# Performance work log

Hardware: AMD Instinct MI355X
Metric: run time of the kernel (lower is better)

Reference implementation:

```python
import jax, jax.numpy as jnp
import numpy as np

B = 16384      # samples
NN = 11        # causal-graph nodes per sample (adult)
D = 4          # per-node raw feature dim (node_dim_max)
F = 32         # dim_input_enc = h_dim_list_enc[0]
EDIM = 4       # edge_dim
NI = 3         # number of intervention features

_BASE_EDGES = np.array([[0,3],[0,4],[1,3],[1,5],[2,5],[0,6],[3,6],[4,7],[5,7],
                        [6,8],[7,8],[2,9],[8,9],[3,10],[6,10],[9,10],[1,10]], dtype=np.int64)


def setup_inputs() -> dict:
    key = jax.random.key(0)
    ks = jax.random.split(key, 14)
    # batched edge index: replicate the 17-edge DAG per sample with node offsets
    off = (np.arange(B) * NN)[:, None]                      # [B,1]
    src = (_BASE_EDGES[:, 0][None, :] + off).reshape(-1).astype(np.int32)  # [E]
    dst = (_BASE_EDGES[:, 1][None, :] + off).reshape(-1).astype(np.int32)
    E = src.shape[0]
    g = lambda k, shp, s: jax.random.normal(k, shp, dtype=jnp.float32) * s
    return {
        'x_input':  g(ks[0], (B, NN * D), 1.0),
        'edge_attr': g(ks[1], (E, EDIM), 1.0),
        'W_emb':   g(ks[2], (NN, D, F), 1.0 / np.sqrt(D)),
        'b_emb':   jnp.zeros((NN, F), jnp.float32),
        'W_pre1':  g(ks[3], (NI, 2 * F + EDIM, F), 1.0 / np.sqrt(2 * F + EDIM)),
        'b_pre1':  jnp.zeros((NI, F), jnp.float32),
        'W_post1': g(ks[4], (NI, 12 * F, F), 1.0 / np.sqrt(12 * F)),
        'b_post1': jnp.zeros((NI, F), jnp.float32),
        'W_pre2':  g(ks[5], (NI, 2 * F + EDIM, F), 1.0 / np.sqrt(2 * F + EDIM)),
        'b_pre2':  jnp.zeros((NI, F), jnp.float32),
        'W_post2': g(ks[6], (NI, 12 * F, 1), 1.0 / np.sqrt(12 * F)),
        'b_post2': jnp.zeros((NI, 1), jnp.float32),
        'W_fc':    g(ks[7], (NI, NN, 1), 1.0 / np.sqrt(NN)),
        'b_fc':    jnp.zeros((NI, 1), jnp.float32),
        'edge_src': jnp.asarray(src),
        'edge_dst': jnp.asarray(dst),
    }


def _pna_conv(h, src, dst, e, Wpre, bpre, Wpost, bpost, cnt_c, mask, amp, att, N):
    # message: pre-MLP over [h_dst, h_src, edge_attr]
    m = jax.nn.relu(jnp.concatenate([h[dst], h[src], e], axis=1) @ Wpre + bpre)  # [E,F]
    s = jax.ops.segment_sum(m, dst, num_segments=N)
    mean = s / cnt_c[:, None]
    mean_sq = jax.ops.segment_sum(m * m, dst, num_segments=N) / cnt_c[:, None]
    std = jnp.sqrt(jax.nn.relu(mean_sq - mean * mean) + 1e-5)
    mn = jnp.where(mask[:, None], jax.ops.segment_min(m, dst, num_segments=N), 0.0)
    mx = jnp.where(mask[:, None], jax.ops.segment_max(m, dst, num_segments=N), 0.0)
    agg = jnp.concatenate([mean, mn, mx, std], axis=1)                 # [N,4F]
    scaled = jnp.concatenate([agg, agg * amp[:, None], agg * att[:, None]], axis=1)  # [N,12F]
    return scaled @ Wpost + bpost


def reference(x_input, edge_attr, W_emb, b_emb,
              W_pre1, b_pre1, W_post1, b_post1,
              W_pre2, b_pre2, W_post2, b_post2,
              W_fc, b_fc, edge_src, edge_dst):
    N = B * NN
    # encoder embeddings: per-node linear + relu (shared across interventions)
    X = x_input.reshape(B, NN, D)
    H = jax.nn.relu(jnp.einsum('bnd,ndf->bnf', X, W_emb) + b_emb).reshape(N, F)
    # degree stats for PNA scalers (in-degree)
    cnt = jax.ops.segment_sum(jnp.ones_like(edge_dst, dtype=jnp.float32), edge_dst, num_segments=N)
    mask = cnt > 0
    cnt_c = jnp.maximum(cnt, 1.0)
    logd = jnp.log1p(jnp.maximum(cnt, 1.0))
    avg_log = jnp.mean(logd)
    amp = logd / avg_log
    att = avg_log / logd
    outs = []
    for i in range(NI):
        h1 = jax.nn.relu(_pna_conv(H, edge_src, edge_dst, edge_attr,
                                   W_pre1[i], b_pre1[i], W_post1[i], b_post1[i],
                                   cnt_c, mask, amp, att, N))
        h2 = _pna_conv(h1, edge_src, edge_dst, edge_attr,
                       W_pre2[i], b_pre2[i], W_post2[i], b_post2[i],
                       cnt_c, mask, amp, att, N)            # [N,1]
        p = jax.nn.sigmoid(h2)                               # get_prob=True
        pm = p.reshape(B, NN).mean(axis=0)                   # return_mean=True -> [11]
        outs.append(pm @ W_fc[i] + b_fc[i])                  # [1]
    # padded sum over interventions == concatenation when inter_features == intervention_features
    return jnp.concatenate(outs)[None, :]                    # [1, NI]
```

## Files before the change

### kernel.cpp

```cpp
#include <hip/hip_runtime.h>
#include <math.h>

#define B_TOT   16384
#define SB      6
#define TPB     512

#define SSTRIDE 1652
#define OFF_H   0
#define OFF_EA  396
#define OFF_H1  464
#define OFF_AGG 860
#define OFF_TD  OFF_AGG
#define OFF_TS  (OFF_AGG + 396)
#define OFF_A4  600
#define OFF_A10 640
#define WLDS    (SB * SSTRIDE)

#define LW_B4   0
#define LW_H1C  32
#define LW_V1C1 64
#define LW_V10  160
#define LW_V4   288
#define LW_C42  320
#define LW_TSC  324
#define LW_BP1  356
#define LW_EA1  388
#define LW_EA2  516
#define LW_WC1  644
#define LTAB    3716

#define OFF_PACC (WLDS + LTAB)
#define LDS_FLOATS (WLDS + LTAB + 16)
#define AVG_LOG 0.9976091242438673f

#define G_WC1  0
#define G_W10  3072
#define G_W4   7168
#define G_SM   8192
#define WTAB   8548
#define WS_TAB 64

__constant__ int C_ESRC[17] = {0,0,1,1,2,0,3,4,5,6,7,2,8,3,6,9,1};
__constant__ int C1EA[6] = {0,3,5,7,9,11};
__constant__ int C1EB[6] = {2,4,6,8,10,12};
__constant__ int C1N[6]  = {3,5,6,7,8,9};

#define FMA16(a, wb, u) do { \
    float4 w0_ = *(const float4*)(wb); \
    float4 w1_ = *(const float4*)((wb) + 32); \
    float4 w2_ = *(const float4*)((wb) + 64); \
    float4 w3_ = *(const float4*)((wb) + 96); \
    u.x = fmaf(a.x, w0_.x, u.x); u.y = fmaf(a.x, w0_.y, u.y); u.z = fmaf(a.x, w0_.z, u.z); u.w = fmaf(a.x, w0_.w, u.w); \
    u.x = fmaf(a.y, w1_.x, u.x); u.y = fmaf(a.y, w1_.y, u.y); u.z = fmaf(a.y, w1_.z, u.z); u.w = fmaf(a.y, w1_.w, u.w); \
    u.x = fmaf(a.z, w2_.x, u.x); u.y = fmaf(a.z, w2_.y, u.y); u.z = fmaf(a.z, w2_.z, u.z); u.w = fmaf(a.z, w2_.w, u.w); \
    u.x = fmaf(a.w, w3_.x, u.x); u.y = fmaf(a.w, w3_.y, u.y); u.z = fmaf(a.w, w3_.z, u.z); u.w = fmaf(a.w, w3_.w, u.w); \
} while (0)

#define MSG(e_, m_) do { \
    const float4 ev_ = *(const float4*)(S + OFF_EA + (e_) * 4); \
    const float4 ts_ = *(const float4*)(S + OFF_TS + C_ESRC[(e_)] * 36 + f); \
    m_.x = base.x + ts_.x; m_.y = base.y + ts_.y; m_.z = base.z + ts_.z; m_.w = base.w + ts_.w; \
    m_.x = fmaf(ev_.x, w0.x, m_.x); m_.y = fmaf(ev_.x, w0.y, m_.y); m_.z = fmaf(ev_.x, w0.z, m_.z); m_.w = fmaf(ev_.x, w0.w, m_.w); \
    m_.x = fmaf(ev_.y, w1.x, m_.x); m_.y = fmaf(ev_.y, w1.y, m_.y); m_.z = fmaf(ev_.y, w1.z, m_.z); m_.w = fmaf(ev_.y, w1.w, m_.w); \
    m_.x = fmaf(ev_.z, w2.x, m_.x); m_.y = fmaf(ev_.z, w2.y, m_.y); m_.z = fmaf(ev_.z, w2.z, m_.z); m_.w = fmaf(ev_.z, w2.w, m_.w); \
    m_.x = fmaf(ev_.w, w3.x, m_.x); m_.y = fmaf(ev_.w, w3.y, m_.y); m_.z = fmaf(ev_.w, w3.z, m_.z); m_.w = fmaf(ev_.w, w3.w, m_.w); \
    m_.x = fmaxf(m_.x, 0.f); m_.y = fmaxf(m_.y, 0.f); m_.z = fmaxf(m_.z, 0.f); m_.w = fmaxf(m_.w, 0.f); \
} while (0)

static __device__ __forceinline__ float coef3(const float* __restrict__ W1, int r, int fcol, float amp, float att)
{
    return W1[r * 32 + fcol] + amp * W1[(128 + r) * 32 + fcol] + att * W1[(256 + r) * 32 + fcol];
}
static __device__ __forceinline__ float coef3s(const float* __restrict__ W2, int r, float amp, float att)
{
    return W2[r] + amp * W2[128 + r] + att * W2[256 + r];
}

extern "C" __global__ void pna_fold(const float* __restrict__ W_post1, const float* __restrict__ b_post1,
                                    const float* __restrict__ W_post2, const float* __restrict__ b_post2,
                                    const float* __restrict__ W_pre2,  float* __restrict__ ws)
{
    const int t0 = blockIdx.x * blockDim.x + threadIdx.x;
    const int NT = gridDim.x * blockDim.x;
    const float l1 = log1pf(1.f), l2 = log1pf(2.f), l4 = log1pf(4.f);
    const float amp1 = l1 / AVG_LOG, att1 = AVG_LOG / l1;
    const float amp2 = l2 / AVG_LOG, att2 = AVG_LOG / l2;
    const float amp4 = l4 / AVG_LOG, att4 = AVG_LOG / l4;
    const float SIG0 = 0.0031622776601683794f;

    for (int idx = t0; idx < 3 * WTAB; idx += NT) {
        const int i = idx / WTAB, off = idx % WTAB;
        const float* W1 = W_post1 + i * 384 * 32;
        const float* W2 = W_post2 + i * 384;
        float val = 0.f;
        if (off < 3072) {
            const int j = off >> 5, fcol = off & 31, sub = j >> 5, jj = j & 31;
            if (sub == 0)      val = coef3(W1, jj, fcol, amp2, att2) + 2.f * coef3(W1, 64 + jj, fcol, amp2, att2);
            else if (sub == 1) val = coef3(W1, 32 + jj, fcol, amp2, att2) - coef3(W1, 64 + jj, fcol, amp2, att2);
            else               val = coef3(W1, 96 + jj, fcol, amp2, att2);
        } else if (off < 7168) {
            const int rr = off - 3072;
            val = coef3(W1, rr >> 5, rr & 31, amp4, att4);
        } else if (off < 8192) {
            const int rr = off - 7168, jj = rr >> 5, fcol = rr & 31;
            val = coef3(W1, jj, fcol, amp1, att1) + coef3(W1, 32 + jj, fcol, amp1, att1)
                + coef3(W1, 64 + jj, fcol, amp1, att1);
        } else if (off < 8224) {
            const int fcol = off - 8192;
            float ssum = 0.f;
            for (int jj = 0; jj < 32; ++jj) ssum += coef3(W1, 96 + jj, fcol, amp1, att1);
            val = b_post1[i * 32 + fcol] + SIG0 * ssum;
        } else if (off < 8256) {
            const int fcol = off - 8224;
            float ssum = 0.f;
            for (int jj = 0; jj < 32; ++jj) ssum += coef3(W1, 96 + jj, fcol, amp1, att1);
            val = fmaxf(b_post1[i * 32 + fcol] + SIG0 * ssum, 0.f);
        } else if (off < 8352) {
            const int j = off - 8256, sub = j >> 5, jj = j & 31;
            if (sub == 0)      val = coef3s(W2, jj, amp2, att2) + 2.f * coef3s(W2, 64 + jj, amp2, att2);
            else if (sub == 1) val = coef3s(W2, 32 + jj, amp2, att2) - coef3s(W2, 64 + jj, amp2, att2);
            else               val = coef3s(W2, 96 + jj, amp2, att2);
        } else if (off < 8480) {
            val = coef3s(W2, off - 8352, amp4, att4);
        } else if (off < 8512) {
            const int jj = off - 8480;
            val = coef3s(W2, jj, amp1, att1) + coef3s(W2, 32 + jj, amp1, att1) + coef3s(W2, 64 + jj, amp1, att1);
        } else if (off == 8512) {
            float ssum = 0.f;
            for (int jj = 0; jj < 32; ++jj) ssum += coef3s(W2, 96 + jj, amp1, att1);
            val = SIG0 * ssum;
        } else if (off >= 8516 && off < 8548) {
            const int fcol = off - 8516;
            const float* Wp2 = W_pre2 + i * 2176;
            float acc = 0.f;
            for (int k = 0; k < 32; ++k) {
                float ssum = 0.f;
                for (int jj = 0; jj < 32; ++jj) ssum += coef3(W1, 96 + jj, k, amp1, att1);
                const float h1c = fmaxf(b_post1[i * 32 + k] + SIG0 * ssum, 0.f);
                acc = fmaf(h1c, Wp2[(32 + k) * 32 + fcol], acc);
            }
            val = acc;
        }
        ws[WS_TAB + idx] = val;
    }
    if (t0 < 40) ws[t0] = 0.f;
    if (t0 >= 40 && t0 < 43) {
        const int i = t0 - 40;
        const float* W2 = W_post2 + i * 384;
        float ssum = 0.f;
        for (int jj = 0; jj < 32; ++jj) ssum += coef3s(W2, 96 + jj, amp1, att1);
        ws[40 + i] = 1.f / (1.f + expf(-(b_post2[i] + SIG0 * ssum)));
    }
}

template<int PASS>
static __device__ __forceinline__ void conv_T(float* lds, const float* wl, int nsamp, int w, int lane,
                                              int hoff, const float* __restrict__ Wp,
                                              const float* __restrict__ bp)
{
    const int ty = w & 1;
    const int f0 = (w >> 1) * 8;
    int s, n, tasks;
    if (ty == 0)            { tasks = nsamp * 8;  s = lane >> 3;  n = 3 + (lane & 7); }
    else if (PASS == 0)     { tasks = nsamp * 10; s = lane / 10;  n = lane % 10; }
    else                    { tasks = nsamp * 7;  s = lane / 7;   n = 3 + lane % 7; }
    const bool act = lane < tasks;
    if (!act) { s = 0; n = 3; }
    const float* Hrow = lds + s * SSTRIDE + hoff + n * 36;
    const float* wbase = Wp + ty * 32 * 32 + f0;
    float acc[8];
#pragma unroll
    for (int f = 0; f < 8; f++) acc[f] = ty ? 0.f : bp[f0 + f];
#pragma unroll
    for (int kq = 0; kq < 8; kq++) {
        float4 a = *(const float4*)(Hrow + kq * 4);
#pragma unroll
        for (int kk = 0; kk < 4; kk++) {
            float av = (kk == 0) ? a.x : (kk == 1) ? a.y : (kk == 2) ? a.z : a.w;
            const float* wr = wbase + (kq * 4 + kk) * 32;
#pragma unroll
            for (int f = 0; f < 8; f++) acc[f] = fmaf(av, wr[f], acc[f]);
        }
    }
    float* T = lds + s * SSTRIDE + (ty ? OFF_TS : OFF_TD) + n * 36 + f0;
    if (act) {
        *(float4*)(T + 0) = make_float4(acc[0], acc[1], acc[2], acc[3]);
        *(float4*)(T + 4) = make_float4(acc[4], acc[5], acc[6], acc[7]);
    }
    if (PASS == 1 && ty == 1) {
        if (lane < nsamp * 3) {
            const int cs = lane / 3, cn = lane % 3;
            float* Tc = lds + cs * SSTRIDE + OFF_TS + cn * 36 + f0;
            *(float4*)(Tc)     = *(const float4*)(wl + LW_TSC + f0);
            *(float4*)(Tc + 4) = *(const float4*)(wl + LW_TSC + f0 + 4);
        }
    }
}

template<int CONV2>
static __device__ __forceinline__ void fused_conv(float* lds, const float* wl, int nsamp,
                                                  int w, int lane, float b2, float* pacc)
{
    const bool act = lane < nsamp * 8;
    const int l = act ? lane : 0;
    const int s = l >> 3, q = l & 7, f = q * 4;
    float* S = lds + s * SSTRIDE;
    const float* WE = wl + (CONV2 ? LW_EA2 : LW_EA1) + f;
    const float4 w0 = *(const float4*)(WE);
    const float4 w1 = *(const float4*)(WE + 32);
    const float4 w2 = *(const float4*)(WE + 64);
    const float4 w3 = *(const float4*)(WE + 96);

    float4 r0 = make_float4(0.f,0.f,0.f,0.f), r1 = r0, r2 = r0, r3 = r0;
    float u = 0.f;

    if (w < 6) {
        const int n = C1N[w];
        float4 base = *(const float4*)(S + OFF_TD + n * 36 + f);
        float4 ma, mb;
        MSG(C1EA[w], ma);
        MSG(C1EB[w], mb);
        r0.x = (ma.x + mb.x) * 0.5f; r0.y = (ma.y + mb.y) * 0.5f;
        r0.z = (ma.z + mb.z) * 0.5f; r0.w = (ma.w + mb.w) * 0.5f;
        r1.x = fminf(ma.x, mb.x); r1.y = fminf(ma.y, mb.y);
        r1.z = fminf(ma.z, mb.z); r1.w = fminf(ma.w, mb.w);
        float4 msq;
        msq.x = fmaf(mb.x, mb.x, ma.x * ma.x) * 0.5f;
        msq.y = fmaf(mb.y, mb.y, ma.y * ma.y) * 0.5f;
        msq.z = fmaf(mb.z, mb.z, ma.z * ma.z) * 0.5f;
        msq.w = fmaf(mb.w, mb.w, ma.w * ma.w) * 0.5f;
        r2.x = sqrtf(fmaxf(msq.x - r0.x * r0.x, 0.f) + 1e-5f);
        r2.y = sqrtf(fmaxf(msq.y - r0.y * r0.y, 0.f) + 1e-5f);
        r2.z = sqrtf(fmaxf(msq.z - r0.z * r0.z, 0.f) + 1e-5f);
        r2.w = sqrtf(fmaxf(msq.w - r0.w * r0.w, 0.f) + 1e-5f);
        if (CONV2) {
            const float* V = wl + LW_V1C1 + f;
            const float4 v0 = *(const float4*)(V);
            const float4 v1 = *(const float4*)(V + 32);
            const float4 v2 = *(const float4*)(V + 64);
            u = fmaf(r0.x, v0.x, fmaf(r0.y, v0.y, fmaf(r0.z, v0.z, r0.w * v0.w)));
            u = fmaf(r1.x, v1.x, fmaf(r1.y, v1.y, fmaf(r1.z, v1.z, fmaf(r1.w, v1.w, u))));
            u = fmaf(r2.x, v2.x, fmaf(r2.y, v2.y, fmaf(r2.z, v2.z, fmaf(r2.w, v2.w, u))));
        }
    } else if (w == 6) {
        float4 base = *(const float4*)(S + OFF_TD + 4 * 36 + f);
        float4 m;
        MSG(1, m);
        r0 = m;
        if (CONV2) {
            const float4 v0 = *(const float4*)(wl + LW_V4 + f);
            u = fmaf(m.x, v0.x, fmaf(m.y, v0.y, fmaf(m.z, v0.z, m.w * v0.w)));
        }
    } else {
        float4 base = *(const float4*)(S + OFF_TD + 10 * 36 + f);
        float4 sum = make_float4(0.f,0.f,0.f,0.f), sq = sum;
        float4 mn = make_float4(1e30f,1e30f,1e30f,1e30f);
        float4 mx = make_float4(-1e30f,-1e30f,-1e30f,-1e30f);
#pragma unroll
        for (int e = 13; e <= 16; ++e) {
            float4 m;
            MSG(e, m);
            sum.x += m.x; sum.y += m.y; sum.z += m.z; sum.w += m.w;
            sq.x = fmaf(m.x, m.x, sq.x); sq.y = fmaf(m.y, m.y, sq.y);
            sq.z = fmaf(m.z, m.z, sq.z); sq.w = fmaf(m.w, m.w, sq.w);
            mn.x = fminf(mn.x, m.x); mn.y = fminf(mn.y, m.y); mn.z = fminf(mn.z, m.z); mn.w = fminf(mn.w, m.w);
            mx.x = fmaxf(mx.x, m.x); mx.y = fmaxf(mx.y, m.y); mx.z = fmaxf(mx.z, m.z); mx.w = fmaxf(mx.w, m.w);
        }
        r0.x = sum.x * 0.25f; r0.y = sum.y * 0.25f; r0.z = sum.z * 0.25f; r0.w = sum.w * 0.25f;
        r1 = mn; r2 = mx;
        float4 msq = make_float4(sq.x * 0.25f, sq.y * 0.25f, sq.z * 0.25f, sq.w * 0.25f);
        r3.x = sqrtf(fmaxf(msq.x - r0.x * r0.x, 0.f) + 1e-5f);
        r3.y = sqrtf(fmaxf(msq.y - r0.y * r0.y, 0.f) + 1e-5f);
        r3.z = sqrtf(fmaxf(msq.z - r0.z * r0.z, 0.f) + 1e-5f);
        r3.w = sqrtf(fmaxf(msq.w - r0.w * r0.w, 0.f) + 1e-5f);
        if (CONV2) {
            const float* V = wl + LW_V10 + f;
            const float4 v0 = *(const float4*)(V);
            const float4 v1 = *(const float4*)(V + 32);
            const float4 v2 = *(const float4*)(V + 64);
            const float4 v3 = *(const float4*)(V + 96);
            u = fmaf(r0.x, v0.x, fmaf(r0.y, v0.y, fmaf(r0.z, v0.z, r0.w * v0.w)));
            u = fmaf(r1.x, v1.x, fmaf(r1.y, v1.y, fmaf(r1.z, v1.z, fmaf(r1.w, v1.w, u))));
            u = fmaf(r2.x, v2.x, fmaf(r2.y, v2.y, fmaf(r2.z, v2.z, fmaf(r2.w, v2.w, u))));
            u = fmaf(r3.x, v3.x, fmaf(r3.y, v3.y, fmaf(r3.z, v3.z, fmaf(r3.w, v3.w, u))));
        }
    }

    if (!CONV2) {
        __syncthreads();
        if (act) {
            if (w < 6) {
                float* A = S + OFF_AGG + w * 100;
                *(float4*)(A + f) = r0; *(float4*)(A + 32 + f) = r1; *(float4*)(A + 64 + f) = r2;
            } else if (w == 6) {
                *(float4*)(S + OFF_AGG + OFF_A4 + f) = r0;
            } else {
                float* A = S + OFF_AGG + OFF_A10;
                *(float4*)(A + f) = r0; *(float4*)(A + 32 + f) = r1;
                *(float4*)(A + 64 + f) = r2; *(float4*)(A + 96 + f) = r3;
            }
        }
    } else {
        u += __shfl_xor(u, 1);
        u += __shfl_xor(u, 2);
        u += __shfl_xor(u, 4);
        if (act && q == 0) {
            const float extra = (w == 6) ? wl[LW_C42] : 0.f;
            const int node = (w < 6) ? C1N[w] : (w == 6 ? 4 : 10);
            const float p = 1.f / (1.f + expf(-(u + b2 + extra)));
            atomicAdd(pacc + node, p);
        }
    }
}

static __device__ __forceinline__ void post1_new(float* lds, const float* wl, int nsamp, int w, int lane,
                                                 const float* __restrict__ tabg)
{
    const bool act = lane < nsamp * 8;
    const int l = act ? lane : 0;
    const int s = l >> 3, q = l & 7;
    if (w < 6) {
        const float* A = lds + s * SSTRIDE + OFF_AGG + w * 100;
        const float* W = wl + LW_WC1 + q * 4;
        float4 u = make_float4(0.f,0.f,0.f,0.f);
#pragma unroll 2
        for (int jq = 0; jq < 24; ++jq) {
            float4 a = *(const float4*)(A + jq * 4);
            FMA16(a, W + jq * 128, u);
        }
        if (act) {
            const float4 b = *(const float4*)(wl + LW_BP1 + q * 4);
            float4 o;
            o.x = fmaxf(u.x + b.x, 0.f); o.y = fmaxf(u.y + b.y, 0.f);
            o.z = fmaxf(u.z + b.z, 0.f); o.w = fmaxf(u.w + b.w, 0.f);
            *(float4*)(lds + s * SSTRIDE + OFF_H1 + C1N[w] * 36 + q * 4) = o;
        }
    } else if (w == 7) {
        const float* A = lds + s * SSTRIDE + OFF_AGG + OFF_A10;
        const float* W = tabg + G_W10 + q * 4;
        float4 u = make_float4(0.f,0.f,0.f,0.f);
#pragma unroll 2
        for (int jq = 0; jq < 32; ++jq) {
            float4 a = *(const float4*)(A + jq * 4);
            FMA16(a, W + jq * 128, u);
        }
        if (act) {
            const float4 b = *(const float4*)(wl + LW_BP1 + q * 4);
            float4 o;
            o.x = fmaxf(u.x + b.x, 0.f); o.y = fmaxf(u.y + b.y, 0.f);
            o.z = fmaxf(u.z + b.z, 0.f); o.w = fmaxf(u.w + b.w, 0.f);
            *(float4*)(lds + s * SSTRIDE + OFF_H1 + 10 * 36 + q * 4) = o;
        }
    } else {
        const float* A = lds + s * SSTRIDE + OFF_AGG + OFF_A4;
        const float* W = tabg + G_W4 + q * 4;
        float4 u = make_float4(0.f,0.f,0.f,0.f);
#pragma unroll
        for (int jq = 0; jq < 8; ++jq) {
            float4 a = *(const float4*)(A + jq * 4);
            FMA16(a, W + jq * 128, u);
        }
        if (act) {
            const float4 b = *(const float4*)(wl + LW_B4 + q * 4);
            float4 o;
            o.x = fmaxf(u.x + b.x, 0.f); o.y = fmaxf(u.y + b.y, 0.f);
            o.z = fmaxf(u.z + b.z, 0.f); o.w = fmaxf(u.w + b.w, 0.f);
            *(float4*)(lds + s * SSTRIDE + OFF_H1 + 4 * 36 + q * 4) = o;
        }
    }
}

extern "C" __global__ void __launch_bounds__(TPB, 4)
pna_main(const float* __restrict__ x_input, const float* __restrict__ edge_attr,
         const float* __restrict__ W_emb,  const float* __restrict__ b_emb,
         const float* __restrict__ W_pre1, const float* __restrict__ b_pre1,
         const float* __restrict__ b_post1,
         const float* __restrict__ W_pre2, const float* __restrict__ b_pre2,
         const float* __restrict__ b_post2,
         const float* __restrict__ wstab,  float* __restrict__ gacc)
{
    extern __shared__ float lds[];
    const int tid = threadIdx.x;
    const int w = __builtin_amdgcn_readfirstlane(tid >> 6);
    const int lane = tid & 63;
    const int s0 = blockIdx.x * SB;
    const int nsamp = min(SB, B_TOT - s0);
    float* wl = lds + WLDS;
    float* pacc = lds + OFF_PACC;

    if (tid < 16) pacc[tid] = 0.f;

    for (int t = tid; t < nsamp * 68; t += TPB)
        lds[(t / 68) * SSTRIDE + OFF_EA + (t % 68)] = edge_attr[(size_t)s0 * 68 + t];

    for (int t = tid; t < nsamp * 352; t += TPB) {
        const int s = t / 352, r = t % 352, n = r >> 5, f = r & 31;
        const float* Xs = x_input + (size_t)(s0 + s) * 44 + n * 4;
        const float* We = W_emb + (n * 4) * 32 + f;
        float v = b_emb[n * 32 + f];
        v = fmaf(Xs[0], We[0],  v);
        v = fmaf(Xs[1], We[32], v);
        v = fmaf(Xs[2], We[64], v);
        v = fmaf(Xs[3], We[96], v);
        lds[s * SSTRIDE + OFF_H + n * 36 + f] = fmaxf(v, 0.f);
    }
    __syncthreads();

    for (int i = 0; i < 3; i++) {
        const float* tab = wstab + i * WTAB;
        for (int t = tid; t < 768; t += TPB)
            ((float4*)(wl + LW_WC1))[t] = ((const float4*)(tab + G_WC1))[t];
        if (tid < 89)       ((float4*)wl)[tid] = ((const float4*)(tab + G_SM))[tid];
        else if (tid < 97)  ((float4*)(wl + LW_BP1))[tid - 89] = ((const float4*)(b_post1 + i * 32))[tid - 89];
        else if (tid < 129) ((float4*)(wl + LW_EA1))[tid - 97] = ((const float4*)(W_pre1 + i * 2176 + 2048))[tid - 97];
        else if (tid < 161) ((float4*)(wl + LW_EA2))[tid - 129] = ((const float4*)(W_pre2 + i * 2176 + 2048))[tid - 129];

        conv_T<0>(lds, wl, nsamp, w, lane, OFF_H, W_pre1 + i * 2176, b_pre1 + i * 32);
        __syncthreads();
        fused_conv<0>(lds, wl, nsamp, w, lane, 0.f, pacc);
        __syncthreads();
        post1_new(lds, wl, nsamp, w, lane, tab);
        __syncthreads();
        conv_T<1>(lds, wl, nsamp, w, lane, OFF_H1, W_pre2 + i * 2176, b_pre2 + i * 32);
        __syncthreads();
        fused_conv<1>(lds, wl, nsamp, w, lane, b_post2[i], pacc);
        __syncthreads();
        if (tid < 11) {
            atomicAdd(gacc + i * 11 + tid, pacc[tid]);
            pacc[tid] = 0.f;
        }
    }
}

extern "C" __global__ void pna_final(const float* __restrict__ ws,
                                     const float* __restrict__ W_fc,
                                     const float* __restrict__ b_fc,
                                     float* __restrict__ out)
{
    const int i = threadIdx.x;
    if (i < 3) {
        float acc = 0.f;
        for (int n = 0; n < 11; n++)
            acc = fmaf(ws[i * 11 + n] * (1.f / 16384.f), W_fc[i * 11 + n], acc);
        const float pc = ws[40 + i];
        const float wsum = W_fc[i * 11 + 0] + W_fc[i * 11 + 1] + W_fc[i * 11 + 2];
        out[i] = acc + pc * wsum + b_fc[i];
    }
}

extern "C" void kernel_launch(void* const* d_in, const int* in_sizes, int n_in,
                              void* d_out, int out_size, void* d_ws, size_t ws_size,
                              hipStream_t stream)
{
    (void)in_sizes; (void)n_in; (void)out_size; (void)ws_size;
    const float* x_input   = (const float*)d_in[0];
    const float* edge_attr = (const float*)d_in[1];
    const float* W_emb     = (const float*)d_in[2];
    const float* b_emb     = (const float*)d_in[3];
    const float* W_pre1    = (const float*)d_in[4];
    const float* b_pre1    = (const float*)d_in[5];
    const float* W_post1   = (const float*)d_in[6];
    const float* b_post1   = (const float*)d_in[7];
    const float* W_pre2    = (const float*)d_in[8];
    const float* b_pre2    = (const float*)d_in[9];
    const float* W_post2   = (const float*)d_in[10];
    const float* b_post2   = (const float*)d_in[11];
    const float* W_fc      = (const float*)d_in[12];
    const float* b_fc      = (const float*)d_in[13];
    float* ws  = (float*)d_ws;
    float* out = (float*)d_out;

    hipLaunchKernelGGL(pna_fold, dim3(64), dim3(512), 0, stream,
                       W_post1, b_post1, W_post2, b_post2, W_pre2, ws);
    const int grid = (B_TOT + SB - 1) / SB;
    const size_t shmem = (size_t)LDS_FLOATS * sizeof(float);
    hipLaunchKernelGGL(pna_main, dim3(grid), dim3(TPB), shmem, stream,
                       x_input, edge_attr, W_emb, b_emb,
                       W_pre1, b_pre1, b_post1,
                       W_pre2, b_pre2, b_post2,
                       ws + WS_TAB, ws);
    hipLaunchKernelGGL(pna_final, dim3(1), dim3(64), 0, stream, ws, W_fc, b_fc, out);
}
```

Before: 331.3 us.

## Precompute edge-attribute projections in conv_T and read post1 weights from global

Measured after the change: 410.6 us. 1.24x slower.

```diff
diff --git a/kernel.cpp b/kernel.cpp
--- a/kernel.cpp
+++ b/kernel.cpp
@@ -24,13 +24,12 @@
 #define LW_C42  320
 #define LW_TSC  324
 #define LW_BP1  356
-#define LW_EA1  388
-#define LW_EA2  516
-#define LW_WC1  644
-#define LTAB    3716
-
-#define OFF_PACC (WLDS + LTAB)
-#define LDS_FLOATS (WLDS + LTAB + 16)
+#define LTAB    388
+
+#define EATSTRIDE 548
+#define OFF_EAT  (WLDS + LTAB)
+#define OFF_PACC (OFF_EAT + SB * EATSTRIDE)
+#define LDS_FLOATS (OFF_PACC + 16)
 #define AVG_LOG 0.9976091242438673f
 
 #define G_WC1  0
@@ -57,14 +56,12 @@
 } while (0)
 
 #define MSG(e_, m_) do { \
-    const float4 ev_ = *(const float4*)(S + OFF_EA + (e_) * 4); \
     const float4 ts_ = *(const float4*)(S + OFF_TS + C_ESRC[(e_)] * 36 + f); \
-    m_.x = base.x + ts_.x; m_.y = base.y + ts_.y; m_.z = base.z + ts_.z; m_.w = base.w + ts_.w; \
-    m_.x = fmaf(ev_.x, w0.x, m_.x); m_.y = fmaf(ev_.x, w0.y, m_.y); m_.z = fmaf(ev_.x, w0.z, m_.z); m_.w = fmaf(ev_.x, w0.w, m_.w); \
-    m_.x = fmaf(ev_.y, w1.x, m_.x); m_.y = fmaf(ev_.y, w1.y, m_.y); m_.z = fmaf(ev_.y, w1.z, m_.z); m_.w = fmaf(ev_.y, w1.w, m_.w); \
-    m_.x = fmaf(ev_.z, w2.x, m_.x); m_.y = fmaf(ev_.z, w2.y, m_.y); m_.z = fmaf(ev_.z, w2.z, m_.z); m_.w = fmaf(ev_.z, w2.w, m_.w); \
-    m_.x = fmaf(ev_.w, w3.x, m_.x); m_.y = fmaf(ev_.w, w3.y, m_.y); m_.z = fmaf(ev_.w, w3.z, m_.z); m_.w = fmaf(ev_.w, w3.w, m_.w); \
-    m_.x = fmaxf(m_.x, 0.f); m_.y = fmaxf(m_.y, 0.f); m_.z = fmaxf(m_.z, 0.f); m_.w = fmaxf(m_.w, 0.f); \
+    const float4 ea_ = *(const float4*)(EAT_s + (e_) * 32 + f); \
+    m_.x = fmaxf(base.x + ts_.x + ea_.x, 0.f); \
+    m_.y = fmaxf(base.y + ts_.y + ea_.y, 0.f); \
+    m_.z = fmaxf(base.z + ts_.z + ea_.z, 0.f); \
+    m_.w = fmaxf(base.w + ts_.w + ea_.w, 0.f); \
 } while (0)
 
 static __device__ __forceinline__ float coef3(const float* __restrict__ W1, int r, int fcol, float amp, float att)
@@ -195,6 +192,24 @@
             *(float4*)(Tc + 4) = *(const float4*)(wl + LW_TSC + f0 + 4);
         }
     }
+    const int tid2 = (w << 6) | lane;
+    for (int t = tid2; t < nsamp * 136; t += TPB) {
+        const int s2 = t / 136, r2 = t - s2 * 136, e2 = r2 >> 3, fo = (r2 & 7) * 4;
+        const float4 ev = *(const float4*)(lds + s2 * SSTRIDE + OFF_EA + e2 * 4);
+        const float4 wa = *(const float4*)(Wp + 2048 + fo);
+        const float4 wb = *(const float4*)(Wp + 2080 + fo);
+        const float4 wc = *(const float4*)(Wp + 2112 + fo);
+        const float4 wd = *(const float4*)(Wp + 2144 + fo);
+        float4 t4;
+        t4.x = ev.x * wa.x; t4.y = ev.x * wa.y; t4.z = ev.x * wa.z; t4.w = ev.x * wa.w;
+        t4.x = fmaf(ev.y, wb.x, t4.x); t4.y = fmaf(ev.y, wb.y, t4.y);
+        t4.z = fmaf(ev.y, wb.z, t4.z); t4.w = fmaf(ev.y, wb.w, t4.w);
+        t4.x = fmaf(ev.z, wc.x, t4.x); t4.y = fmaf(ev.z, wc.y, t4.y);
+        t4.z = fmaf(ev.z, wc.z, t4.z); t4.w = fmaf(ev.z, wc.w, t4.w);
+        t4.x = fmaf(ev.w, wd.x, t4.x); t4.y = fmaf(ev.w, wd.y, t4.y);
+        t4.z = fmaf(ev.w, wd.z, t4.z); t4.w = fmaf(ev.w, wd.w, t4.w);
+        *(float4*)(lds + OFF_EAT + s2 * EATSTRIDE + e2 * 32 + fo) = t4;
+    }
 }
 
 template<int CONV2>
@@ -205,11 +220,7 @@
     const int l = act ? lane : 0;
     const int s = l >> 3, q = l & 7, f = q * 4;
     float* S = lds + s * SSTRIDE;
-    const float* WE = wl + (CONV2 ? LW_EA2 : LW_EA1) + f;
-    const float4 w0 = *(const float4*)(WE);
-    const float4 w1 = *(const float4*)(WE + 32);
-    const float4 w2 = *(const float4*)(WE + 64);
-    const float4 w3 = *(const float4*)(WE + 96);
+    const float* EAT_s = lds + OFF_EAT + s * EATSTRIDE;
 
     float4 r0 = make_float4(0.f,0.f,0.f,0.f), r1 = r0, r2 = r0, r3 = r0;
     float u = 0.f;
@@ -321,7 +332,7 @@
     const int s = l >> 3, q = l & 7;
     if (w < 6) {
         const float* A = lds + s * SSTRIDE + OFF_AGG + w * 100;
-        const float* W = wl + LW_WC1 + q * 4;
+        const float* W = tabg + G_WC1 + q * 4;
         float4 u = make_float4(0.f,0.f,0.f,0.f);
 #pragma unroll 2
         for (int jq = 0; jq < 24; ++jq) {
@@ -408,12 +419,8 @@
 
     for (int i = 0; i < 3; i++) {
         const float* tab = wstab + i * WTAB;
-        for (int t = tid; t < 768; t += TPB)
-            ((float4*)(wl + LW_WC1))[t] = ((const float4*)(tab + G_WC1))[t];
-        if (tid < 89)       ((float4*)wl)[tid] = ((const float4*)(tab + G_SM))[tid];
-        else if (tid < 97)  ((float4*)(wl + LW_BP1))[tid - 89] = ((const float4*)(b_post1 + i * 32))[tid - 89];
-        else if (tid < 129) ((float4*)(wl + LW_EA1))[tid - 97] = ((const float4*)(W_pre1 + i * 2176 + 2048))[tid - 97];
-        else if (tid < 161) ((float4*)(wl + LW_EA2))[tid - 129] = ((const float4*)(W_pre2 + i * 2176 + 2048))[tid - 129];
+        if (tid < 89)      ((float4*)wl)[tid] = ((const float4*)(tab + G_SM))[tid];
+        else if (tid < 97) ((float4*)(wl + LW_BP1))[tid - 89] = ((const float4*)(b_post1 + i * 32))[tid - 89];
 
         conv_T<0>(lds, wl, nsamp, w, lane, OFF_H, W_pre1 + i * 2176, b_pre1 + i * 32);
         __syncthreads();
```
